# Kernel optimization log

Measured on AMD Instinct MI355X. Metric: run time of the kernel, lower is better.

## Reference

```python
import jax, jax.numpy as jnp
import numpy as np

H = 1024
V = 50257
N = 4096
IGNORE_INDEX = -100


def setup_inputs() -> dict:
    key = jax.random.key(0)
    k1, k2, k3 = jax.random.split(key, 3)
    x = jax.random.normal(k1, (N, H), dtype=jnp.float32)
    weight = jax.random.normal(k2, (V, H), dtype=jnp.float32) * (H ** -0.5)
    target = jax.random.randint(k3, (N,), 0, V, dtype=jnp.int32)
    return {"x": x, "target": target, "weight": weight}


def reference(x, target, weight):
    # Fused LM head + cross-entropy (math-equivalent unfused form).
    logits = jnp.einsum("nh,vh->nv", x, weight)  # [N, V]
    logz = jax.nn.logsumexp(logits, axis=-1)     # [N]
    safe_tgt = jnp.where(target == IGNORE_INDEX, 0, target)
    picked = jnp.take_along_axis(logits, safe_tgt[:, None].astype(jnp.int32), axis=-1)[:, 0]
    valid = target != IGNORE_INDEX
    per_tok = jnp.where(valid, logz - picked, 0.0)
    n_valid = jnp.maximum(jnp.sum(valid), 1)
    return jnp.sum(per_tok) / n_valid.astype(per_tok.dtype)
```

## Files before the change

kernel.cpp:

```cpp
#include <hip/hip_runtime.h>
#include <hip/hip_bf16.h>
#include <hip/hip_fp8.h>

#define N_TOK 4096
#define H_DIM 1024
#define V_DIM 50257
#define IGNORE_IDX (-100)

#define BM 128
#define BN 128
#define BK 128
#define NSTEP (H_DIM / BK)
#define NCHUNK ((V_DIM + BN - 1) / BN)

#define LDT 72

typedef __attribute__((ext_vector_type(8))) short bf16x8;
typedef __attribute__((ext_vector_type(4))) float f32x4;
typedef long longx2 __attribute__((ext_vector_type(2)));

union Pack8 { __hip_bfloat162 h2[4]; int4 v; };

__device__ __forceinline__ void gload16(const void* g, void* l) {
    __builtin_amdgcn_global_load_lds(
        (const __attribute__((address_space(1))) unsigned int*)g,
        (__attribute__((address_space(3))) unsigned int*)l,
        16, 0, 0);
}

__device__ __forceinline__ int pack4_fp8(float a, float b, float c, float d) {
#if __has_builtin(__builtin_amdgcn_cvt_pk_fp8_f32)
    int w = __builtin_amdgcn_cvt_pk_fp8_f32(a, b, 0, false);
    w = __builtin_amdgcn_cvt_pk_fp8_f32(c, d, w, true);
    return w;
#else
    __hip_fp8_e4m3 q0(a), q1(b), q2(c), q3(d);
    return (int)q0.__x | ((int)q1.__x << 8) | ((int)q2.__x << 16) | ((int)q3.__x << 24);
#endif
}

__global__ __launch_bounds__(256) void cvt_x8p_kernel(const float* __restrict__ x,
                                                      unsigned char* __restrict__ xb8) {
    size_t E = (size_t)blockIdx.x * 256 + threadIdx.x;
    int o = (int)(E & 7);
    size_t blk = E >> 3;
    const float* s = x + (blk << 7) + ((size_t)(o >> 2) << 6) + ((o & 3) << 3);
    float4 f0 = *(const float4*)(s);
    float4 f1 = *(const float4*)(s + 4);
    float4 f2 = *(const float4*)(s + 32);
    float4 f3 = *(const float4*)(s + 36);
    int4 out;
    out.x = pack4_fp8(f0.x, f0.y, f0.z, f0.w);
    out.y = pack4_fp8(f1.x, f1.y, f1.z, f1.w);
    out.z = pack4_fp8(f2.x, f2.y, f2.z, f2.w);
    out.w = pack4_fp8(f3.x, f3.y, f3.z, f3.w);
    reinterpret_cast<int4*>(xb8)[E] = out;
}

__global__ __launch_bounds__(256) void cvt_w8p_kernel(const float* __restrict__ W,
                                                      unsigned char* __restrict__ Wb8) {
    const size_t total = (size_t)V_DIM * H_DIM / 16;
    size_t stride = (size_t)gridDim.x * 256;
    for (size_t E = (size_t)blockIdx.x * 256 + threadIdx.x; E < total; E += stride) {
        int o = (int)(E & 7);
        size_t blk = E >> 3;
        const float* s = W + (blk << 7) + ((size_t)(o >> 2) << 6) + ((o & 3) << 3);
        float4 f0 = *(const float4*)(s);
        float4 f1 = *(const float4*)(s + 4);
        float4 f2 = *(const float4*)(s + 32);
        float4 f3 = *(const float4*)(s + 36);
        int4 out;
        out.x = pack4_fp8(f0.x, f0.y, f0.z, f0.w);
        out.y = pack4_fp8(f1.x, f1.y, f1.z, f1.w);
        out.z = pack4_fp8(f2.x, f2.y, f2.z, f2.w);
        out.w = pack4_fp8(f3.x, f3.y, f3.z, f3.w);
        reinterpret_cast<int4*>(Wb8)[E] = out;
    }
}

__global__ __launch_bounds__(256, 4) void ce_gemm_fp8(
        const unsigned char* __restrict__ xb8,
        const unsigned char* __restrict__ Wb8,
        const int* __restrict__ tgt,
        float2* __restrict__ partials,
        float* __restrict__ picked) {
    __shared__ __align__(16) char lA[BM * BK];
    __shared__ __align__(16) char lB[BN * BK];
    __shared__ float2 mergebuf[BM][2];
    __shared__ int ltgt[BM];

    const int tid  = threadIdx.x;
    const int mb   = blockIdx.x;
    const int vb   = blockIdx.y;
    const int rbase = mb * BM;
    const int cbase = vb * BN;
    const int lane = tid & 63;
    const int wid  = tid >> 6;
    const int wr   = wid >> 1;
    const int wc   = wid & 1;
    const int l15  = lane & 15;
    const int lg   = lane >> 4;

    if (tid < BM) ltgt[tid] = tgt[rbase + tid];

    const unsigned char* srcA[4];
    const unsigned char* srcB[4];
    #pragma unroll
    for (int it = 0; it < 4; ++it) {
        int G = it * 256 + tid;
        int r = G >> 3, g = G & 7;
        int gs = g ^ (r & 7);
        srcA[it] = xb8 + (size_t)(rbase + r) * H_DIM + gs * 16;
        int vr = cbase + r; if (vr >= V_DIM) vr = V_DIM - 1;
        srcB[it] = Wb8 + (size_t)vr * H_DIM + gs * 16;
    }

    int aoffb[4], boffb[4];
    #pragma unroll
    for (int m = 0; m < 4; ++m) {
        int r = wr * 64 + m * 16 + l15;
        aoffb[m] = r * 128 + ((lg ^ (r & 7)) << 4);
    }
    #pragma unroll
    for (int n = 0; n < 4; ++n) {
        int r = wc * 64 + n * 16 + l15;
        boffb[n] = r * 128 + ((lg ^ (r & 7)) << 4);
    }

    f32x4 acc[4][4] = {};

    for (int s = 0; s < NSTEP; ++s) {
        const int k0 = s * BK;
        __syncthreads();
        #pragma unroll
        for (int it = 0; it < 4; ++it) {
            gload16(srcA[it] + k0, lA + (it * 256 + wid * 64) * 16);
            gload16(srcB[it] + k0, lB + (it * 256 + wid * 64) * 16);
        }
        __syncthreads();

        longx2 va[4][2], vb[4][2];
        #pragma unroll
        for (int m = 0; m < 4; ++m) {
            va[m][0] = *reinterpret_cast<const longx2*>(lA + aoffb[m]);
            va[m][1] = *reinterpret_cast<const longx2*>(lA + (aoffb[m] ^ 64));
        }
        #pragma unroll
        for (int n = 0; n < 4; ++n) {
            vb[n][0] = *reinterpret_cast<const longx2*>(lB + boffb[n]);
            vb[n][1] = *reinterpret_cast<const longx2*>(lB + (boffb[n] ^ 64));
        }
        #pragma unroll
        for (int kk = 0; kk < 4; ++kk)
            #pragma unroll
            for (int m = 0; m < 4; ++m)
                #pragma unroll
                for (int n = 0; n < 4; ++n)
                    acc[m][n] = __builtin_amdgcn_mfma_f32_16x16x32_fp8_fp8(
                        va[m][kk >> 1][kk & 1], vb[n][kk >> 1][kk & 1], acc[m][n], 0, 0, 0);
    }

    #pragma unroll
    for (int m = 0; m < 4; ++m) {
        #pragma unroll
        for (int j = 0; j < 4; ++j) {
            int rl = wr * 64 + m * 16 + lg * 4 + j;
            int tg = ltgt[rl];
            float v4[4];
            float vmax = -INFINITY;
            #pragma unroll
            for (int n = 0; n < 4; ++n) {
                int cg = cbase + wc * 64 + n * 16 + l15;
                float val = acc[m][n][j];
                bool ok = cg < V_DIM;
                v4[n] = ok ? val : -INFINITY;
                if (ok && tg == cg) picked[rbase + rl] = val;
                vmax = fmaxf(vmax, v4[n]);
            }
            #pragma unroll
            for (int msk = 1; msk <= 8; msk <<= 1)
                vmax = fmaxf(vmax, __shfl_xor(vmax, msk));
            float ssum = 0.f;
            #pragma unroll
            for (int n = 0; n < 4; ++n)
                ssum += (v4[n] == -INFINITY) ? 0.f : __expf(v4[n] - vmax);
            #pragma unroll
            for (int msk = 1; msk <= 8; msk <<= 1)
                ssum += __shfl_xor(ssum, msk);
            if (l15 == 0) mergebuf[rl][wc] = make_float2(vmax, ssum);
        }
    }
    __syncthreads();
    if (tid < BM) {
        float2 p0 = mergebuf[tid][0], p1 = mergebuf[tid][1];
        float M = fmaxf(p0.x, p1.x);
        float sm = 0.f;
        if (p0.x > -INFINITY) sm += p0.y * __expf(p0.x - M);
        if (p1.x > -INFINITY) sm += p1.y * __expf(p1.x - M);
        partials[(size_t)(rbase + tid) * NCHUNK + vb] = make_float2(M, sm);
    }
}

__global__ __launch_bounds__(256) void cvt_x_kernel(const float* __restrict__ x,
                                                    __hip_bfloat16* __restrict__ xb) {
    size_t e = (size_t)blockIdx.x * 256 + threadIdx.x;
    const float4* s = reinterpret_cast<const float4*>(x) + e * 2;
    float4 a = s[0], b = s[1];
    Pack8 p;
    p.h2[0] = __float22bfloat162_rn(make_float2(a.x, a.y));
    p.h2[1] = __float22bfloat162_rn(make_float2(a.z, a.w));
    p.h2[2] = __float22bfloat162_rn(make_float2(b.x, b.y));
    p.h2[3] = __float22bfloat162_rn(make_float2(b.z, b.w));
    reinterpret_cast<int4*>(xb)[e] = p.v;
}

__global__ __launch_bounds__(256) void ce_gemm_kernel(
        const __hip_bfloat16* __restrict__ xb, const float* __restrict__ W,
        const int* __restrict__ tgt, float2* __restrict__ partials, float* __restrict__ picked) {
    __shared__ __hip_bfloat16 lA[BM * LDT];
    __shared__ __hip_bfloat16 lB[BN * LDT];
    __shared__ float2 mergebuf[BM][2];
    __shared__ int ltgt[BM];
    const int tid = threadIdx.x, mb = blockIdx.x, vb = blockIdx.y;
    const int rbase = mb * BM, cbase = vb * BN;
    const int lane = tid & 63, wid = tid >> 6;
    const int wr = wid >> 1, wc = wid & 1, l15 = lane & 15, lg = lane >> 4;
    if (tid < BM) ltgt[tid] = tgt[rbase + tid];
    f32x4 acc[4][4] = {};
    for (int s = 0; s < H_DIM / 64; ++s) {
        const int k0 = s * 64;
        __syncthreads();
        #pragma unroll
        for (int it = 0; it < 4; ++it) {
            int e = it * 256 + tid, r = e >> 3, c8 = e & 7;
            int4 v = *reinterpret_cast<const int4*>(xb + (size_t)(rbase + r) * H_DIM + k0 + c8 * 8);
            *reinterpret_cast<int4*>(&lA[r * LDT + c8 * 8]) = v;
        }
        #pragma unroll
        for (int it = 0; it < 4; ++it) {
            int e = it * 256 + tid, r = e >> 3, c8 = e & 7;
            int v = cbase + r; if (v >= V_DIM) v = V_DIM - 1;
            const float4* src = reinterpret_cast<const float4*>(W + (size_t)v * H_DIM + k0 + c8 * 8);
            float4 f0 = src[0], f1 = src[1];
            Pack8 p;
            p.h2[0] = __float22bfloat162_rn(make_float2(f0.x, f0.y));
            p.h2[1] = __float22bfloat162_rn(make_float2(f0.z, f0.w));
            p.h2[2] = __float22bfloat162_rn(make_float2(f1.x, f1.y));
            p.h2[3] = __float22bfloat162_rn(make_float2(f1.z, f1.w));
            *reinterpret_cast<int4*>(&lB[r * LDT + c8 * 8]) = p.v;
        }
        __syncthreads();
        #pragma unroll
        for (int kk = 0; kk < 2; ++kk) {
            bf16x8 af[4], bfr[4];
            #pragma unroll
            for (int m = 0; m < 4; ++m)
                af[m] = *reinterpret_cast<const bf16x8*>(&lA[(wr * 64 + m * 16 + l15) * LDT + kk * 32 + lg * 8]);
            #pragma unroll
            for (int n = 0; n < 4; ++n)
                bfr[n] = *reinterpret_cast<const bf16x8*>(&lB[(wc * 64 + n * 16 + l15) * LDT + kk * 32 + lg * 8]);
            #pragma unroll
            for (int m = 0; m < 4; ++m)
                #pragma unroll
                for (int n = 0; n < 4; ++n)
                    acc[m][n] = __builtin_amdgcn_mfma_f32_16x16x32_bf16(af[m], bfr[n], acc[m][n], 0, 0, 0);
        }
    }
    #pragma unroll
    for (int m = 0; m < 4; ++m) {
        #pragma unroll
        for (int j = 0; j < 4; ++j) {
            int rl = wr * 64 + m * 16 + lg * 4 + j;
            int tg = ltgt[rl];
            float v4[4]; float vmax = -INFINITY;
            #pragma unroll
            for (int n = 0; n < 4; ++n) {
                int cg = cbase + wc * 64 + n * 16 + l15;
                float val = acc[m][n][j];
                bool ok = cg < V_DIM;
                v4[n] = ok ? val : -INFINITY;
                if (ok && tg == cg) picked[rbase + rl] = val;
                vmax = fmaxf(vmax, v4[n]);
            }
            #pragma unroll
            for (int msk = 1; msk <= 8; msk <<= 1) vmax = fmaxf(vmax, __shfl_xor(vmax, msk));
            float ssum = 0.f;
            #pragma unroll
            for (int n = 0; n < 4; ++n) ssum += (v4[n] == -INFINITY) ? 0.f : __expf(v4[n] - vmax);
            #pragma unroll
            for (int msk = 1; msk <= 8; msk <<= 1) ssum += __shfl_xor(ssum, msk);
            if (l15 == 0) mergebuf[rl][wc] = make_float2(vmax, ssum);
        }
    }
    __syncthreads();
    if (tid < BM) {
        float2 p0 = mergebuf[tid][0], p1 = mergebuf[tid][1];
        float M = fmaxf(p0.x, p1.x);
        float sm = 0.f;
        if (p0.x > -INFINITY) sm += p0.y * __expf(p0.x - M);
        if (p1.x > -INFINITY) sm += p1.y * __expf(p1.x - M);
        partials[(size_t)(rbase + tid) * NCHUNK + vb] = make_float2(M, sm);
    }
}

__global__ __launch_bounds__(256) void ce_combine_kernel(
        const float2* __restrict__ partials, const float* __restrict__ picked,
        const int* __restrict__ tgt, float2* __restrict__ blockSums, int nchunk) {
    __shared__ float2 wsum[4];
    int tid = threadIdx.x, lane = tid & 63, wave = tid >> 6;
    int w = blockIdx.x * 4 + wave;
    float sum = 0.f, cnt = 0.f;
    for (int row = w; row < N_TOK; row += 256) {
        float m = -INFINITY, sacc = 0.f;
        for (int c = lane; c < nchunk; c += 64) {
            float2 p = partials[(size_t)row * nchunk + c];
            float M = fmaxf(m, p.x);
            sacc = sacc * __expf(m - M) + p.y * __expf(p.x - M);
            m = M;
        }
        #pragma unroll
        for (int msk = 1; msk < 64; msk <<= 1) {
            float om = __shfl_xor(m, msk), os = __shfl_xor(sacc, msk);
            float M = fmaxf(m, om);
            sacc = sacc * __expf(m - M) + os * __expf(om - M);
            m = M;
        }
        if (lane == 0) {
            int t = tgt[row];
            if (t != IGNORE_IDX) { sum += (m + __logf(sacc)) - picked[row]; cnt += 1.f; }
        }
    }
    if (lane == 0) wsum[wave] = make_float2(sum, cnt);
    __syncthreads();
    if (tid == 0) {
        float S = 0.f, C = 0.f;
        #pragma unroll
        for (int i = 0; i < 4; ++i) { S += wsum[i].x; C += wsum[i].y; }
        blockSums[blockIdx.x] = make_float2(S, C);
    }
}

__global__ void ce_final_kernel(const float2* __restrict__ blockSums, float* __restrict__ out) {
    int lane = threadIdx.x;
    float2 p = blockSums[lane];
    float S = p.x, C = p.y;
    #pragma unroll
    for (int msk = 1; msk < 64; msk <<= 1) { S += __shfl_xor(S, msk); C += __shfl_xor(C, msk); }
    if (lane == 0) out[0] = S / fmaxf(C, 1.f);
}

extern "C" void kernel_launch(void* const* d_in, const int* in_sizes, int n_in,
                              void* d_out, int out_size, void* d_ws, size_t ws_size,
                              hipStream_t stream) {
    const float* x   = (const float*)d_in[0];
    const int*   tgt = (const int*)d_in[1];
    const float* W   = (const float*)d_in[2];
    float* out = (float*)d_out;
    char* ws = (char*)d_ws;

    if (ws_size >= ((size_t)80 << 20)) {
        unsigned char* xb8 = (unsigned char*)ws;
        unsigned char* Wb8 = (unsigned char*)(ws + ((size_t)8 << 20));
        float2* partials   = (float2*)(ws + ((size_t)60 << 20));
        float*  picked     = (float*)(ws + ((size_t)76 << 20));
        float2* blockSums  = (float2*)(ws + ((size_t)77 << 20));

        cvt_x8p_kernel<<<(N_TOK * H_DIM) / (256 * 16), 256, 0, stream>>>(x, xb8);
        cvt_w8p_kernel<<<2048, 256, 0, stream>>>(W, Wb8);
        dim3 grid(N_TOK / BM, NCHUNK);
        ce_gemm_fp8<<<grid, 256, 0, stream>>>(xb8, Wb8, tgt, partials, picked);
        ce_combine_kernel<<<64, 256, 0, stream>>>(partials, picked, tgt, blockSums, NCHUNK);
        ce_final_kernel<<<1, 64, 0, stream>>>(blockSums, out);
    } else {
        __hip_bfloat16* xb = (__hip_bfloat16*)ws;
        float2* partials   = (float2*)(ws + (8u << 20));
        float*  picked     = (float*)(ws + (21u << 20));
        float2* blockSums  = (float2*)(ws + (21u << 20) + (64u << 10));

        cvt_x_kernel<<<(N_TOK * H_DIM) / (256 * 8), 256, 0, stream>>>(x, xb);
        dim3 grid(N_TOK / BM, NCHUNK);
        ce_gemm_kernel<<<grid, 256, 0, stream>>>(xb, W, tgt, partials, picked);
        ce_combine_kernel<<<64, 256, 0, stream>>>(partials, picked, tgt, blockSums, NCHUNK);
        ce_final_kernel<<<1, 64, 0, stream>>>(blockSums, out);
    }
}
```

Measured before the change: 399.3 us.

## Widen FP8 GEMM tile to 128x256 with 8 waves per block

Doubles the vocab tile width of the FP8 GEMM to 256 columns and runs 512 threads (8 waves, 2x4 layout) per block, so each block reuses its x tile across twice as many vocab rows. The per-block merge of softmax partials is extended to four wave-columns with an online max/sum combine. This halves the number of partial chunks written and the redundant x tile loads, at the cost of more LDS per block and possibly lower occupancy. The bf16 fallback path keeps 128-wide tiles via a separate chunk count.

New measurement: 402.6 us. No clear change (+0.8%).

```diff
diff --git a/kernel.cpp b/kernel.cpp
--- a/kernel.cpp
+++ b/kernel.cpp
@@ -8,12 +8,13 @@
 #define IGNORE_IDX (-100)
 
 #define BM 128
-#define BN 128
+#define BN 256
 #define BK 128
 #define NSTEP (H_DIM / BK)
 #define NCHUNK ((V_DIM + BN - 1) / BN)
 
 #define LDT 72
+#define NCHUNK_FB ((V_DIM + 127) / 128)
 
 typedef __attribute__((ext_vector_type(8))) short bf16x8;
 typedef __attribute__((ext_vector_type(4))) float f32x4;
@@ -78,7 +79,7 @@
     }
 }
 
-__global__ __launch_bounds__(256, 4) void ce_gemm_fp8(
+__global__ __launch_bounds__(512, 4) void ce_gemm_fp8(
         const unsigned char* __restrict__ xb8,
         const unsigned char* __restrict__ Wb8,
         const int* __restrict__ tgt,
@@ -86,7 +87,7 @@
         float* __restrict__ picked) {
     __shared__ __align__(16) char lA[BM * BK];
     __shared__ __align__(16) char lB[BN * BK];
-    __shared__ float2 mergebuf[BM][2];
+    __shared__ float2 mergebuf[BM][4];
     __shared__ int ltgt[BM];
 
     const int tid  = threadIdx.x;
@@ -96,23 +97,29 @@
     const int cbase = vb * BN;
     const int lane = tid & 63;
     const int wid  = tid >> 6;
-    const int wr   = wid >> 1;
-    const int wc   = wid & 1;
+    const int wr   = wid >> 2;
+    const int wc   = wid & 3;
     const int l15  = lane & 15;
     const int lg   = lane >> 4;
 
     if (tid < BM) ltgt[tid] = tgt[rbase + tid];
 
-    const unsigned char* srcA[4];
+    const unsigned char* srcA[2];
     const unsigned char* srcB[4];
     #pragma unroll
-    for (int it = 0; it < 4; ++it) {
-        int G = it * 256 + tid;
+    for (int q = 0; q < 2; ++q) {
+        int G = q * 512 + tid;
         int r = G >> 3, g = G & 7;
         int gs = g ^ (r & 7);
-        srcA[it] = xb8 + (size_t)(rbase + r) * H_DIM + gs * 16;
+        srcA[q] = xb8 + (size_t)(rbase + r) * H_DIM + gs * 16;
+    }
+    #pragma unroll
+    for (int q = 0; q < 4; ++q) {
+        int G = q * 512 + tid;
+        int r = G >> 3, g = G & 7;
+        int gs = g ^ (r & 7);
         int vr = cbase + r; if (vr >= V_DIM) vr = V_DIM - 1;
-        srcB[it] = Wb8 + (size_t)vr * H_DIM + gs * 16;
+        srcB[q] = Wb8 + (size_t)vr * H_DIM + gs * 16;
     }
 
     int aoffb[4], boffb[4];
@@ -132,11 +139,11 @@
     for (int s = 0; s < NSTEP; ++s) {
         const int k0 = s * BK;
         __syncthreads();
-        #pragma unroll
-        for (int it = 0; it < 4; ++it) {
-            gload16(srcA[it] + k0, lA + (it * 256 + wid * 64) * 16);
-            gload16(srcB[it] + k0, lB + (it * 256 + wid * 64) * 16);
-        }
+        gload16(srcA[0] + k0, lA + (wid * 64) * 16);
+        gload16(srcA[1] + k0, lA + (512 + wid * 64) * 16);
+        #pragma unroll
+        for (int q = 0; q < 4; ++q)
+            gload16(srcB[q] + k0, lB + (q * 512 + wid * 64) * 16);
         __syncthreads();
 
         longx2 va[4][2], vb[4][2];
@@ -192,11 +199,16 @@
     }
     __syncthreads();
     if (tid < BM) {
-        float2 p0 = mergebuf[tid][0], p1 = mergebuf[tid][1];
-        float M = fmaxf(p0.x, p1.x);
-        float sm = 0.f;
-        if (p0.x > -INFINITY) sm += p0.y * __expf(p0.x - M);
-        if (p1.x > -INFINITY) sm += p1.y * __expf(p1.x - M);
+        float M = -INFINITY, sm = 0.f;
+        #pragma unroll
+        for (int c = 0; c < 4; ++c) {
+            float2 p = mergebuf[tid][c];
+            if (p.x > -INFINITY) {
+                float M2 = fmaxf(M, p.x);
+                sm = sm * __expf(M - M2) + p.y * __expf(p.x - M2);
+                M = M2;
+            }
+        }
         partials[(size_t)(rbase + tid) * NCHUNK + vb] = make_float2(M, sm);
     }
 }
@@ -218,11 +230,11 @@
         const __hip_bfloat16* __restrict__ xb, const float* __restrict__ W,
         const int* __restrict__ tgt, float2* __restrict__ partials, float* __restrict__ picked) {
     __shared__ __hip_bfloat16 lA[BM * LDT];
-    __shared__ __hip_bfloat16 lB[BN * LDT];
+    __shared__ __hip_bfloat16 lB[128 * LDT];
     __shared__ float2 mergebuf[BM][2];
     __shared__ int ltgt[BM];
     const int tid = threadIdx.x, mb = blockIdx.x, vb = blockIdx.y;
-    const int rbase = mb * BM, cbase = vb * BN;
+    const int rbase = mb * BM, cbase = vb * 128;
     const int lane = tid & 63, wid = tid >> 6;
     const int wr = wid >> 1, wc = wid & 1, l15 = lane & 15, lg = lane >> 4;
     if (tid < BM) ltgt[tid] = tgt[rbase + tid];
@@ -299,7 +311,7 @@
         float sm = 0.f;
         if (p0.x > -INFINITY) sm += p0.y * __expf(p0.x - M);
         if (p1.x > -INFINITY) sm += p1.y * __expf(p1.x - M);
-        partials[(size_t)(rbase + tid) * NCHUNK + vb] = make_float2(M, sm);
+        partials[(size_t)(rbase + tid) * NCHUNK_FB + vb] = make_float2(M, sm);
     }
 }
 
@@ -368,7 +380,7 @@
         cvt_x8p_kernel<<<(N_TOK * H_DIM) / (256 * 16), 256, 0, stream>>>(x, xb8);
         cvt_w8p_kernel<<<2048, 256, 0, stream>>>(W, Wb8);
         dim3 grid(N_TOK / BM, NCHUNK);
-        ce_gemm_fp8<<<grid, 256, 0, stream>>>(xb8, Wb8, tgt, partials, picked);
+        ce_gemm_fp8<<<grid, 512, 0, stream>>>(xb8, Wb8, tgt, partials, picked);
         ce_combine_kernel<<<64, 256, 0, stream>>>(partials, picked, tgt, blockSums, NCHUNK);
         ce_final_kernel<<<1, 64, 0, stream>>>(blockSums, out);
     } else {
@@ -378,9 +390,9 @@
         float2* blockSums  = (float2*)(ws + (21u << 20) + (64u << 10));
 
         cvt_x_kernel<<<(N_TOK * H_DIM) / (256 * 8), 256, 0, stream>>>(x, xb);
-        dim3 grid(N_TOK / BM, NCHUNK);
+        dim3 grid(N_TOK / BM, NCHUNK_FB);
         ce_gemm_kernel<<<grid, 256, 0, stream>>>(xb, W, tgt, partials, picked);
-        ce_combine_kernel<<<64, 256, 0, stream>>>(partials, picked, tgt, blockSums, NCHUNK);
+        ce_combine_kernel<<<64, 256, 0, stream>>>(partials, picked, tgt, blockSums, NCHUNK_FB);
         ce_final_kernel<<<1, 64, 0, stream>>>(blockSums, out);
     }
 }
```
